# Kernel tuning notes

Measured on AMD Instinct MI355X. Metric: run time of the kernel, lower is better.

Reference implementation:

```python
import jax, jax.numpy as jnp
import numpy as np

M = 16          # max number of instance ids (0 = background)
DELTA_AGG = 0.5
DELTA_DIS = 3.0


def setup_inputs() -> dict:
    key = jax.random.key(0)
    k1, k2 = jax.random.split(key)
    preds = jax.random.normal(k1, (8, 6, 640, 640), dtype=jnp.float32)
    targets = jax.random.randint(k2, (8, 2, 640, 640), 0, M).astype(jnp.int32)
    return {"preds": preds, "targets": targets}


def _seg_sum(vals, ids):
    # vals: [P] or [P, C], ids: [P] -> segment sums with M segments
    return jax.ops.segment_sum(vals, ids, num_segments=M)


def reference(preds, targets):
    N = preds.shape[0]
    sim = preds[:, 2:, :, :].reshape(N, 4, -1).transpose(0, 2, 1)  # N x P x 4
    text = targets[:, 0].reshape(N, -1)                            # N x P
    kern = targets[:, 1].reshape(N, -1)                            # N x P
    P = sim.shape[1]

    seg = jax.vmap(_seg_sum)
    ones = jnp.ones((N, P), sim.dtype)
    cnt_k = seg(ones, kern)                         # N x M kernel pixel counts
    cnt_t = seg(ones, text)                         # N x M text pixel counts
    G = seg(sim, kern) / jnp.maximum(cnt_k, 1.0)[..., None]  # N x M x 4, G_Ki means

    inst = jnp.arange(M)
    valid = (cnt_k > 0) & (cnt_t > 0) & (inst[None, :] >= 1)  # N x M (skip id 0)
    nv = jnp.sum(valid, axis=1)                                # N, number of valid instances

    # ---- aggregation loss: per text pixel, distance to its instance's kernel mean
    G_t = jnp.take_along_axis(G, text[..., None], axis=1)      # N x P x 4
    d = jnp.linalg.norm(sim - G_t, axis=-1) - DELTA_AGG        # N x P
    l = jnp.log(jnp.square(jnp.maximum(d, 0.0)) + 1.0)         # N x P
    l_mean = seg(l, text) / jnp.maximum(cnt_t, 1.0)            # N x M per-instance mean
    agg = jnp.sum(jnp.where(valid, l_mean, 0.0), axis=1) / jnp.maximum(nv, 1)

    # ---- discrimination loss: pairwise distances between valid kernel means
    pair = valid[:, :, None] & valid[:, None, :] & ~jnp.eye(M, dtype=bool)[None]
    sq = jnp.sum(jnp.square(G[:, :, None, :] - G[:, None, :, :]), axis=-1)  # N x M x M
    dist = jnp.sqrt(jnp.where(pair, sq, 1.0))
    lp = jnp.where(pair, jnp.log(jnp.square(jnp.maximum(DELTA_DIS - dist, 0.0)) + 1.0), 0.0)
    dis = jnp.where(nv > 1, 0.5 * jnp.sum(lp, axis=(1, 2)) / jnp.maximum(nv * (nv - 1), 1), 0.0)

    return agg.astype(jnp.float32), dis.astype(jnp.float32)
```

## Files before the change

kernel.cpp:

```cpp
#include <hip/hip_runtime.h>
#include <math.h>

#define NB 8
#define MSEG 16
#define PPIX (640*640)
#define PV4 (PPIX/4)
#define DELTA_AGG 0.5f
#define DELTA_DIS 3.0f

#define OFF_CNT_K 0
#define OFF_CNT_T (NB*MSEG)
#define OFF_G     (2*NB*MSEG)
#define OFF_LSUM  (6*NB*MSEG)
#define WS_FLOATS (7*NB*MSEG)

__device__ __forceinline__ float wave_sum64(float v) {
#pragma unroll
  for (int off = 32; off > 0; off >>= 1) v += __shfl_xor(v, off);
  return v;
}

__global__ __launch_bounds__(256, 2) void pass1_kernel(
    const float* __restrict__ preds, const int* __restrict__ targets,
    float* __restrict__ ws) {
  const int n = blockIdx.y;
  const int tid = threadIdx.x;

  const float4* __restrict__ c0 = (const float4*)(preds + ((size_t)n*6 + 2)*PPIX);
  const float4* __restrict__ c1 = (const float4*)(preds + ((size_t)n*6 + 3)*PPIX);
  const float4* __restrict__ c2 = (const float4*)(preds + ((size_t)n*6 + 4)*PPIX);
  const float4* __restrict__ c3 = (const float4*)(preds + ((size_t)n*6 + 5)*PPIX);
  const int4*  __restrict__ textv = (const int4*)(targets + (size_t)n*2*PPIX);
  const int4*  __restrict__ kernv = (const int4*)(targets + ((size_t)n*2 + 1)*PPIX);

  float s0[MSEG], s1[MSEG], s2[MSEG], s3[MSEG], ck[MSEG], ct[MSEG];
#pragma unroll
  for (int m = 0; m < MSEG; ++m) { s0[m]=0.f; s1[m]=0.f; s2[m]=0.f; s3[m]=0.f; ck[m]=0.f; ct[m]=0.f; }

#define PIX1(K, T, A0, A1, A2, A3)                      \
  _Pragma("unroll")                                     \
  for (int m = 0; m < MSEG; ++m) {                      \
    float fk = ((K) == m) ? 1.0f : 0.0f;                \
    s0[m] = fmaf(fk, (A0), s0[m]);                      \
    s1[m] = fmaf(fk, (A1), s1[m]);                      \
    s2[m] = fmaf(fk, (A2), s2[m]);                      \
    s3[m] = fmaf(fk, (A3), s3[m]);                      \
    ck[m] += fk;                                        \
    ct[m] += ((T) == m) ? 1.0f : 0.0f;                  \
  }

  for (int p = blockIdx.x*256 + tid; p < PV4; p += gridDim.x*256) {
    int4 kk = kernv[p];
    int4 tt = textv[p];
    float4 a = c0[p], b = c1[p], c = c2[p], d = c3[p];
    PIX1(kk.x, tt.x, a.x, b.x, c.x, d.x);
    PIX1(kk.y, tt.y, a.y, b.y, c.y, d.y);
    PIX1(kk.z, tt.z, a.z, b.z, c.z, d.z);
    PIX1(kk.w, tt.w, a.w, b.w, c.w, d.w);
  }
#undef PIX1

#pragma unroll
  for (int m = 0; m < MSEG; ++m) {
    s0[m] = wave_sum64(s0[m]);
    s1[m] = wave_sum64(s1[m]);
    s2[m] = wave_sum64(s2[m]);
    s3[m] = wave_sum64(s3[m]);
    ck[m] = wave_sum64(ck[m]);
    ct[m] = wave_sum64(ct[m]);
  }

  __shared__ float s_red[4][96];
  const int w = tid >> 6, lane = tid & 63;
  if (lane == 0) {
#pragma unroll
    for (int m = 0; m < MSEG; ++m) {
      s_red[w][m*4 + 0] = s0[m];
      s_red[w][m*4 + 1] = s1[m];
      s_red[w][m*4 + 2] = s2[m];
      s_red[w][m*4 + 3] = s3[m];
      s_red[w][64 + m]  = ck[m];
      s_red[w][80 + m]  = ct[m];
    }
  }
  __syncthreads();
  if (tid < 96) {
    float v = s_red[0][tid] + s_red[1][tid] + s_red[2][tid] + s_red[3][tid];
    if (tid < 64)      atomicAdd(&ws[OFF_G + n*64 + tid], v);
    else if (tid < 80) atomicAdd(&ws[OFF_CNT_K + n*MSEG + (tid - 64)], v);
    else               atomicAdd(&ws[OFF_CNT_T + n*MSEG + (tid - 80)], v);
  }
}

__global__ __launch_bounds__(256) void finalize_dis_kernel(
    float* __restrict__ ws, float* __restrict__ out) {
  const int n = blockIdx.x;
  const int tid = threadIdx.x;
  float* cnt_k = ws + OFF_CNT_K + n*MSEG;
  float* cnt_t = ws + OFF_CNT_T + n*MSEG;
  float* G     = ws + OFF_G     + (size_t)n*MSEG*4;

  __shared__ float s_G[MSEG][4];
  __shared__ int   s_valid[MSEG];
  __shared__ int   s_nv;
  __shared__ float red[256];

  if (tid < MSEG*4) {
    int m = tid >> 2;
    float g = G[tid] / fmaxf(cnt_k[m], 1.0f);
    s_G[m][tid & 3] = g;
    G[tid] = g;
  }
  if (tid < MSEG)
    s_valid[tid] = (tid >= 1) && (cnt_k[tid] > 0.f) && (cnt_t[tid] > 0.f);
  __syncthreads();
  if (tid == 0) { int nv = 0; for (int m = 0; m < MSEG; m++) nv += s_valid[m]; s_nv = nv; }

  float lp = 0.f;
  {
    int i = tid >> 4, j = tid & 15;
    if (i != j && s_valid[i] && s_valid[j]) {
      float dx = s_G[i][0] - s_G[j][0];
      float dy = s_G[i][1] - s_G[j][1];
      float dz = s_G[i][2] - s_G[j][2];
      float dw = s_G[i][3] - s_G[j][3];
      float dist = sqrtf(dx*dx + dy*dy + dz*dz + dw*dw);
      float t = fmaxf(DELTA_DIS - dist, 0.f);
      lp = logf(t*t + 1.f);
    }
  }
  red[tid] = lp;
  __syncthreads();
  for (int s = 128; s > 0; s >>= 1) {
    if (tid < s) red[tid] += red[tid + s];
    __syncthreads();
  }
  if (tid == 0) {
    int nv = s_nv;
    float dis = 0.f;
    if (nv > 1) dis = 0.5f * red[0] / (float)(nv * (nv - 1));
    out[NB + n] = dis;
  }
}

__global__ __launch_bounds__(256, 2) void pass2_kernel(
    const float* __restrict__ preds, const int* __restrict__ targets,
    float* __restrict__ ws) {
  const int n = blockIdx.y;
  const int tid = threadIdx.x;

  const float4* __restrict__ c0 = (const float4*)(preds + ((size_t)n*6 + 2)*PPIX);
  const float4* __restrict__ c1 = (const float4*)(preds + ((size_t)n*6 + 3)*PPIX);
  const float4* __restrict__ c2 = (const float4*)(preds + ((size_t)n*6 + 4)*PPIX);
  const float4* __restrict__ c3 = (const float4*)(preds + ((size_t)n*6 + 5)*PPIX);
  const int4*  __restrict__ textv = (const int4*)(targets + (size_t)n*2*PPIX);

  __shared__ float4 s_G[MSEG];
  if (tid < MSEG) s_G[tid] = ((const float4*)(ws + OFF_G + (size_t)n*MSEG*4))[tid];
  __syncthreads();

  float ls[MSEG];
#pragma unroll
  for (int m = 0; m < MSEG; ++m) ls[m] = 0.f;

#define PIX2(T, A0, A1, A2, A3) do {                            \
    float4 g = s_G[(T)];                                        \
    float dx = (A0) - g.x, dy = (A1) - g.y;                     \
    float dz = (A2) - g.z, dw = (A3) - g.w;                     \
    float sq = fmaf(dx, dx, fmaf(dy, dy, fmaf(dz, dz, dw*dw))); \
    float dd = fmaxf(__fsqrt_rn(sq) - DELTA_AGG, 0.f);          \
    float l = __logf(fmaf(dd, dd, 1.f));                        \
    _Pragma("unroll")                                           \
    for (int m = 0; m < MSEG; ++m)                              \
      ls[m] += ((T) == m) ? l : 0.f;                            \
  } while (0)

  for (int p = blockIdx.x*256 + tid; p < PV4; p += gridDim.x*256) {
    int4 tt = textv[p];
    float4 a = c0[p], b = c1[p], c = c2[p], d = c3[p];
    PIX2(tt.x, a.x, b.x, c.x, d.x);
    PIX2(tt.y, a.y, b.y, c.y, d.y);
    PIX2(tt.z, a.z, b.z, c.z, d.z);
    PIX2(tt.w, a.w, b.w, c.w, d.w);
  }
#undef PIX2

#pragma unroll
  for (int m = 0; m < MSEG; ++m) ls[m] = wave_sum64(ls[m]);

  __shared__ float s_red[4][MSEG];
  const int w = tid >> 6, lane = tid & 63;
  if (lane == 0) {
#pragma unroll
    for (int m = 0; m < MSEG; ++m) s_red[w][m] = ls[m];
  }
  __syncthreads();
  if (tid < MSEG) {
    float v = s_red[0][tid] + s_red[1][tid] + s_red[2][tid] + s_red[3][tid];
    atomicAdd(&ws[OFF_LSUM + n*MSEG + tid], v);
  }
}

__global__ __launch_bounds__(64) void finalize_agg_kernel(
    const float* __restrict__ ws, float* __restrict__ out) {
  const int n = blockIdx.x;
  const int tid = threadIdx.x;
  const float* cnt_k = ws + OFF_CNT_K + n*MSEG;
  const float* cnt_t = ws + OFF_CNT_T + n*MSEG;
  const float* lsum  = ws + OFF_LSUM  + n*MSEG;

  float lm = 0.f, vc = 0.f;
  if (tid >= 1 && tid < MSEG) {
    float ck = cnt_k[tid], ct = cnt_t[tid];
    if (ck > 0.f && ct > 0.f) {
      vc = 1.f;
      lm = lsum[tid] / fmaxf(ct, 1.f);
    }
  }
  for (int off = 32; off > 0; off >>= 1) {
    lm += __shfl_down(lm, off);
    vc += __shfl_down(vc, off);
  }
  if (tid == 0) {
    int nv = (int)(vc + 0.5f);
    out[n] = lm / (float)(nv > 1 ? nv : 1);
  }
}

extern "C" void kernel_launch(void* const* d_in, const int* in_sizes, int n_in,
                              void* d_out, int out_size, void* d_ws, size_t ws_size,
                              hipStream_t stream) {
  const float* preds   = (const float*)d_in[0];
  const int*   targets = (const int*)d_in[1];
  float* out = (float*)d_out;
  float* ws  = (float*)d_ws;

  hipMemsetAsync(d_ws, 0, WS_FLOATS * sizeof(float), stream);

  dim3 grid(128, NB);
  pass1_kernel<<<grid, 256, 0, stream>>>(preds, targets, ws);
  finalize_dis_kernel<<<NB, 256, 0, stream>>>(ws, out);
  pass2_kernel<<<grid, 256, 0, stream>>>(preds, targets, ws);
  finalize_agg_kernel<<<NB, 64, 0, stream>>>(ws, out);
}
```

Baseline: 67.32 us.

## Use ballot counts, transpose-style wave reductions and fixed-trip unrolled loops

Pass 1 now counts kernel and text pixels with wave ballots plus popcount instead of per-lane float counters, which removes 32 accumulator registers. Both passes replace per-segment butterfly wave sums with a recursive-halving reduction that shuffles half the accumulators at each step, so the total number of shuffles drops. The grid is reduced to 100 blocks so each thread does exactly 4 fully unrolled iterations. This hardcodes the image size divisibility (100*256*4 == PV4) and raises instruction-level parallelism, at some register pressure cost.

Result: slower. 160.5 us (+138.4%).

```diff
diff --git a/kernel.cpp b/kernel.cpp
--- a/kernel.cpp
+++ b/kernel.cpp
@@ -5,6 +5,8 @@
 #define MSEG 16
 #define PPIX (640*640)
 #define PV4 (PPIX/4)
+#define GRIDX 100
+#define STRIDE (GRIDX*256)
 #define DELTA_AGG 0.5f
 #define DELTA_DIS 3.0f
 
@@ -14,17 +16,12 @@
 #define OFF_LSUM  (6*NB*MSEG)
 #define WS_FLOATS (7*NB*MSEG)
 
-__device__ __forceinline__ float wave_sum64(float v) {
-#pragma unroll
-  for (int off = 32; off > 0; off >>= 1) v += __shfl_xor(v, off);
-  return v;
-}
-
 __global__ __launch_bounds__(256, 2) void pass1_kernel(
     const float* __restrict__ preds, const int* __restrict__ targets,
     float* __restrict__ ws) {
   const int n = blockIdx.y;
   const int tid = threadIdx.x;
+  const int lane = tid & 63, w = tid >> 6;
 
   const float4* __restrict__ c0 = (const float4*)(preds + ((size_t)n*6 + 2)*PPIX);
   const float4* __restrict__ c1 = (const float4*)(preds + ((size_t)n*6 + 3)*PPIX);
@@ -33,23 +30,30 @@
   const int4*  __restrict__ textv = (const int4*)(targets + (size_t)n*2*PPIX);
   const int4*  __restrict__ kernv = (const int4*)(targets + ((size_t)n*2 + 1)*PPIX);
 
-  float s0[MSEG], s1[MSEG], s2[MSEG], s3[MSEG], ck[MSEG], ct[MSEG];
-#pragma unroll
-  for (int m = 0; m < MSEG; ++m) { s0[m]=0.f; s1[m]=0.f; s2[m]=0.f; s3[m]=0.f; ck[m]=0.f; ct[m]=0.f; }
-
-#define PIX1(K, T, A0, A1, A2, A3)                      \
-  _Pragma("unroll")                                     \
-  for (int m = 0; m < MSEG; ++m) {                      \
-    float fk = ((K) == m) ? 1.0f : 0.0f;                \
-    s0[m] = fmaf(fk, (A0), s0[m]);                      \
-    s1[m] = fmaf(fk, (A1), s1[m]);                      \
-    s2[m] = fmaf(fk, (A2), s2[m]);                      \
-    s3[m] = fmaf(fk, (A3), s3[m]);                      \
-    ck[m] += fk;                                        \
-    ct[m] += ((T) == m) ? 1.0f : 0.0f;                  \
-  }
-
-  for (int p = blockIdx.x*256 + tid; p < PV4; p += gridDim.x*256) {
+  float vals[64];
+#pragma unroll
+  for (int v = 0; v < 64; ++v) vals[v] = 0.f;
+  int ckw[MSEG], ctw[MSEG];
+#pragma unroll
+  for (int m = 0; m < MSEG; ++m) { ckw[m] = 0; ctw[m] = 0; }
+
+#define PIX1(K, T, A0, A1, A2, A3)                                  \
+  _Pragma("unroll")                                                 \
+  for (int m = 0; m < MSEG; ++m) {                                  \
+    bool pk = ((K) == m);                                           \
+    ckw[m] += __popcll(__ballot(pk));                               \
+    ctw[m] += __popcll(__ballot((T) == m));                         \
+    float fk = pk ? 1.0f : 0.0f;                                    \
+    vals[0*16+m] = fmaf(fk, (A0), vals[0*16+m]);                    \
+    vals[1*16+m] = fmaf(fk, (A1), vals[1*16+m]);                    \
+    vals[2*16+m] = fmaf(fk, (A2), vals[2*16+m]);                    \
+    vals[3*16+m] = fmaf(fk, (A3), vals[3*16+m]);                    \
+  }
+
+  const int base = blockIdx.x*256 + tid;
+#pragma unroll
+  for (int it = 0; it < 4; ++it) {
+    int p = base + it*STRIDE;
     int4 kk = kernv[p];
     int4 tt = textv[p];
     float4 a = c0[p], b = c1[p], c = c2[p], d = c3[p];
@@ -61,34 +65,34 @@
 #undef PIX1
 
 #pragma unroll
-  for (int m = 0; m < MSEG; ++m) {
-    s0[m] = wave_sum64(s0[m]);
-    s1[m] = wave_sum64(s1[m]);
-    s2[m] = wave_sum64(s2[m]);
-    s3[m] = wave_sum64(s3[m]);
-    ck[m] = wave_sum64(ck[m]);
-    ct[m] = wave_sum64(ct[m]);
-  }
-
-  __shared__ float s_red[4][96];
-  const int w = tid >> 6, lane = tid & 63;
+  for (int s = 0; s < 6; ++s) {
+    const int dist = 32 >> s;
+    const bool hi = (lane & dist) != 0;
+#pragma unroll
+    for (int v = 0; v < (32 >> s); ++v) {
+      float keep = hi ? vals[v + (32 >> s)] : vals[v];
+      float send = hi ? vals[v] : vals[v + (32 >> s)];
+      vals[v] = keep + __shfl_xor(send, dist);
+    }
+  }
+
+  __shared__ float s_vals[4][64];
+  __shared__ int   s_cnt[4][32];
+  s_vals[w][lane] = vals[0];
   if (lane == 0) {
 #pragma unroll
-    for (int m = 0; m < MSEG; ++m) {
-      s_red[w][m*4 + 0] = s0[m];
-      s_red[w][m*4 + 1] = s1[m];
-      s_red[w][m*4 + 2] = s2[m];
-      s_red[w][m*4 + 3] = s3[m];
-      s_red[w][64 + m]  = ck[m];
-      s_red[w][80 + m]  = ct[m];
-    }
-  }
-  __syncthreads();
-  if (tid < 96) {
-    float v = s_red[0][tid] + s_red[1][tid] + s_red[2][tid] + s_red[3][tid];
-    if (tid < 64)      atomicAdd(&ws[OFF_G + n*64 + tid], v);
-    else if (tid < 80) atomicAdd(&ws[OFF_CNT_K + n*MSEG + (tid - 64)], v);
-    else               atomicAdd(&ws[OFF_CNT_T + n*MSEG + (tid - 80)], v);
+    for (int m = 0; m < MSEG; ++m) { s_cnt[w][m] = ckw[m]; s_cnt[w][16+m] = ctw[m]; }
+  }
+  __syncthreads();
+  if (tid < 64) {
+    float v = s_vals[0][tid] + s_vals[1][tid] + s_vals[2][tid] + s_vals[3][tid];
+    int ch = tid >> 4, m = tid & 15;
+    atomicAdd(&ws[OFF_G + n*64 + m*4 + ch], v);
+  } else if (tid < 96) {
+    int i = tid - 64;
+    float v = (float)(s_cnt[0][i] + s_cnt[1][i] + s_cnt[2][i] + s_cnt[3][i]);
+    if (i < 16) atomicAdd(&ws[OFF_CNT_K + n*MSEG + i], v);
+    else        atomicAdd(&ws[OFF_CNT_T + n*MSEG + (i - 16)], v);
   }
 }
 
@@ -148,6 +152,7 @@
     float* __restrict__ ws) {
   const int n = blockIdx.y;
   const int tid = threadIdx.x;
+  const int lane = tid & 63, w = tid >> 6;
 
   const float4* __restrict__ c0 = (const float4*)(preds + ((size_t)n*6 + 2)*PPIX);
   const float4* __restrict__ c1 = (const float4*)(preds + ((size_t)n*6 + 3)*PPIX);
@@ -175,7 +180,10 @@
       ls[m] += ((T) == m) ? l : 0.f;                            \
   } while (0)
 
-  for (int p = blockIdx.x*256 + tid; p < PV4; p += gridDim.x*256) {
+  const int base = blockIdx.x*256 + tid;
+#pragma unroll
+  for (int it = 0; it < 4; ++it) {
+    int p = base + it*STRIDE;
     int4 tt = textv[p];
     float4 a = c0[p], b = c1[p], c = c2[p], d = c3[p];
     PIX2(tt.x, a.x, b.x, c.x, d.x);
@@ -186,19 +194,26 @@
 #undef PIX2
 
 #pragma unroll
-  for (int m = 0; m < MSEG; ++m) ls[m] = wave_sum64(ls[m]);
+  for (int s = 0; s < 4; ++s) {
+    const int dist = 32 >> s;
+    const bool hi = (lane & dist) != 0;
+#pragma unroll
+    for (int v = 0; v < (8 >> s); ++v) {
+      float keep = hi ? ls[v + (8 >> s)] : ls[v];
+      float send = hi ? ls[v] : ls[v + (8 >> s)];
+      ls[v] = keep + __shfl_xor(send, dist);
+    }
+  }
+  float t = ls[0];
+  t += __shfl_xor(t, 2);
+  t += __shfl_xor(t, 1);
 
   __shared__ float s_red[4][MSEG];
-  const int w = tid >> 6, lane = tid & 63;
-  if (lane == 0) {
-#pragma unroll
-    for (int m = 0; m < MSEG; ++m) s_red[w][m] = ls[m];
-  }
-  __syncthreads();
-  if (tid < MSEG) {
-    float v = s_red[0][tid] + s_red[1][tid] + s_red[2][tid] + s_red[3][tid];
-    atomicAdd(&ws[OFF_LSUM + n*MSEG + tid], v);
-  }
+  if ((lane & 3) == 0) s_red[w][lane >> 2] = t;
+  __syncthreads();
+  if (tid < MSEG)
+    atomicAdd(&ws[OFF_LSUM + n*MSEG + tid],
+              s_red[0][tid] + s_red[1][tid] + s_red[2][tid] + s_red[3][tid]);
 }
 
 __global__ __launch_bounds__(64) void finalize_agg_kernel(
@@ -237,7 +252,7 @@
 
   hipMemsetAsync(d_ws, 0, WS_FLOATS * sizeof(float), stream);
 
-  dim3 grid(128, NB);
+  dim3 grid(GRIDX, NB);
   pass1_kernel<<<grid, 256, 0, stream>>>(preds, targets, ws);
   finalize_dis_kernel<<<NB, 256, 0, stream>>>(ws, out);
   pass2_kernel<<<grid, 256, 0, stream>>>(preds, targets, ws);
```

## Replace register one-hot segment sums with LDS atomic histograms

Applied to the files above, without the earlier changes.

Both passes drop the per-thread 16-way one-hot accumulation across 96 (pass1) or 16 (pass2) registers. Each pixel now does shared-memory atomicAdds into per-column bins, with pairs of threads sharing a column. At the end, threads reduce the rows and issue global atomics. The grid becomes a fixed 100 blocks per image, each covering exactly 1024 float4s with no grid-stride loop. This cuts ALU work and register pressure, but adds contention on LDS float atomics and depends on the exact size match (100*1024 == PV4).

Result: slower. 174.6 us (+159.4%).

```diff
diff --git a/kernel.cpp b/kernel.cpp
--- a/kernel.cpp
+++ b/kernel.cpp
@@ -5,6 +5,7 @@
 #define MSEG 16
 #define PPIX (640*640)
 #define PV4 (PPIX/4)
+#define GRIDX 100
 #define DELTA_AGG 0.5f
 #define DELTA_DIS 3.0f
 
@@ -14,17 +15,12 @@
 #define OFF_LSUM  (6*NB*MSEG)
 #define WS_FLOATS (7*NB*MSEG)
 
-__device__ __forceinline__ float wave_sum64(float v) {
-#pragma unroll
-  for (int off = 32; off > 0; off >>= 1) v += __shfl_xor(v, off);
-  return v;
-}
-
-__global__ __launch_bounds__(256, 2) void pass1_kernel(
+__global__ __launch_bounds__(256) void pass1_kernel(
     const float* __restrict__ preds, const int* __restrict__ targets,
     float* __restrict__ ws) {
   const int n = blockIdx.y;
   const int tid = threadIdx.x;
+  const int col = tid >> 1;
 
   const float4* __restrict__ c0 = (const float4*)(preds + ((size_t)n*6 + 2)*PPIX);
   const float4* __restrict__ c1 = (const float4*)(preds + ((size_t)n*6 + 3)*PPIX);
@@ -33,23 +29,28 @@
   const int4*  __restrict__ textv = (const int4*)(targets + (size_t)n*2*PPIX);
   const int4*  __restrict__ kernv = (const int4*)(targets + ((size_t)n*2 + 1)*PPIX);
 
-  float s0[MSEG], s1[MSEG], s2[MSEG], s3[MSEG], ck[MSEG], ct[MSEG];
-#pragma unroll
-  for (int m = 0; m < MSEG; ++m) { s0[m]=0.f; s1[m]=0.f; s2[m]=0.f; s3[m]=0.f; ck[m]=0.f; ct[m]=0.f; }
-
-#define PIX1(K, T, A0, A1, A2, A3)                      \
-  _Pragma("unroll")                                     \
-  for (int m = 0; m < MSEG; ++m) {                      \
-    float fk = ((K) == m) ? 1.0f : 0.0f;                \
-    s0[m] = fmaf(fk, (A0), s0[m]);                      \
-    s1[m] = fmaf(fk, (A1), s1[m]);                      \
-    s2[m] = fmaf(fk, (A2), s2[m]);                      \
-    s3[m] = fmaf(fk, (A3), s3[m]);                      \
-    ck[m] += fk;                                        \
-    ct[m] += ((T) == m) ? 1.0f : 0.0f;                  \
-  }
-
-  for (int p = blockIdx.x*256 + tid; p < PV4; p += gridDim.x*256) {
+  __shared__ float s_acc[6][MSEG][128];
+  {
+    float4* f4 = (float4*)&s_acc[0][0][0];
+#pragma unroll
+    for (int i = 0; i < 12; ++i) f4[tid + i*256] = make_float4(0.f, 0.f, 0.f, 0.f);
+  }
+  __syncthreads();
+
+#define PIX1(K, T, A0, A1, A2, A3) do {          \
+    int k_ = (K), t_ = (T);                      \
+    atomicAdd(&s_acc[0][k_][col], (A0));         \
+    atomicAdd(&s_acc[1][k_][col], (A1));         \
+    atomicAdd(&s_acc[2][k_][col], (A2));         \
+    atomicAdd(&s_acc[3][k_][col], (A3));         \
+    atomicAdd(&s_acc[4][k_][col], 1.0f);         \
+    atomicAdd(&s_acc[5][t_][col], 1.0f);         \
+  } while (0)
+
+  const int base = blockIdx.x*1024 + tid;
+#pragma unroll
+  for (int it = 0; it < 4; ++it) {
+    int p = base + it*256;
     int4 kk = kernv[p];
     int4 tt = textv[p];
     float4 a = c0[p], b = c1[p], c = c2[p], d = c3[p];
@@ -59,36 +60,20 @@
     PIX1(kk.w, tt.w, a.w, b.w, c.w, d.w);
   }
 #undef PIX1
-
-#pragma unroll
-  for (int m = 0; m < MSEG; ++m) {
-    s0[m] = wave_sum64(s0[m]);
-    s1[m] = wave_sum64(s1[m]);
-    s2[m] = wave_sum64(s2[m]);
-    s3[m] = wave_sum64(s3[m]);
-    ck[m] = wave_sum64(ck[m]);
-    ct[m] = wave_sum64(ct[m]);
-  }
-
-  __shared__ float s_red[4][96];
-  const int w = tid >> 6, lane = tid & 63;
-  if (lane == 0) {
-#pragma unroll
-    for (int m = 0; m < MSEG; ++m) {
-      s_red[w][m*4 + 0] = s0[m];
-      s_red[w][m*4 + 1] = s1[m];
-      s_red[w][m*4 + 2] = s2[m];
-      s_red[w][m*4 + 3] = s3[m];
-      s_red[w][64 + m]  = ck[m];
-      s_red[w][80 + m]  = ct[m];
-    }
-  }
-  __syncthreads();
+  __syncthreads();
+
   if (tid < 96) {
-    float v = s_red[0][tid] + s_red[1][tid] + s_red[2][tid] + s_red[3][tid];
-    if (tid < 64)      atomicAdd(&ws[OFF_G + n*64 + tid], v);
-    else if (tid < 80) atomicAdd(&ws[OFF_CNT_K + n*MSEG + (tid - 64)], v);
-    else               atomicAdd(&ws[OFF_CNT_T + n*MSEG + (tid - 80)], v);
+    const int arr = tid >> 4, bin = tid & 15;
+    const float4* row = (const float4*)&s_acc[arr][bin][0];
+    float s = 0.f;
+#pragma unroll
+    for (int i = 0; i < 32; ++i) {
+      float4 v = row[i];
+      s += (v.x + v.y) + (v.z + v.w);
+    }
+    if (arr < 4)       atomicAdd(&ws[OFF_G + n*64 + bin*4 + arr], s);
+    else if (arr == 4) atomicAdd(&ws[OFF_CNT_K + n*MSEG + bin], s);
+    else               atomicAdd(&ws[OFF_CNT_T + n*MSEG + bin], s);
   }
 }
 
@@ -143,11 +128,12 @@
   }
 }
 
-__global__ __launch_bounds__(256, 2) void pass2_kernel(
+__global__ __launch_bounds__(256) void pass2_kernel(
     const float* __restrict__ preds, const int* __restrict__ targets,
     float* __restrict__ ws) {
   const int n = blockIdx.y;
   const int tid = threadIdx.x;
+  const int col = tid >> 1;
 
   const float4* __restrict__ c0 = (const float4*)(preds + ((size_t)n*6 + 2)*PPIX);
   const float4* __restrict__ c1 = (const float4*)(preds + ((size_t)n*6 + 3)*PPIX);
@@ -156,26 +142,30 @@
   const int4*  __restrict__ textv = (const int4*)(targets + (size_t)n*2*PPIX);
 
   __shared__ float4 s_G[MSEG];
+  __shared__ float  s_l[MSEG][128];
   if (tid < MSEG) s_G[tid] = ((const float4*)(ws + OFF_G + (size_t)n*MSEG*4))[tid];
-  __syncthreads();
-
-  float ls[MSEG];
-#pragma unroll
-  for (int m = 0; m < MSEG; ++m) ls[m] = 0.f;
+  {
+    float4* f4 = (float4*)&s_l[0][0];
+#pragma unroll
+    for (int i = 0; i < 2; ++i) f4[tid + i*256] = make_float4(0.f, 0.f, 0.f, 0.f);
+  }
+  __syncthreads();
 
 #define PIX2(T, A0, A1, A2, A3) do {                            \
-    float4 g = s_G[(T)];                                        \
+    int t_ = (T);                                               \
+    float4 g = s_G[t_];                                         \
     float dx = (A0) - g.x, dy = (A1) - g.y;                     \
     float dz = (A2) - g.z, dw = (A3) - g.w;                     \
     float sq = fmaf(dx, dx, fmaf(dy, dy, fmaf(dz, dz, dw*dw))); \
     float dd = fmaxf(__fsqrt_rn(sq) - DELTA_AGG, 0.f);          \
     float l = __logf(fmaf(dd, dd, 1.f));                        \
-    _Pragma("unroll")                                           \
-    for (int m = 0; m < MSEG; ++m)                              \
-      ls[m] += ((T) == m) ? l : 0.f;                            \
+    atomicAdd(&s_l[t_][col], l);                                \
   } while (0)
 
-  for (int p = blockIdx.x*256 + tid; p < PV4; p += gridDim.x*256) {
+  const int base = blockIdx.x*1024 + tid;
+#pragma unroll
+  for (int it = 0; it < 4; ++it) {
+    int p = base + it*256;
     int4 tt = textv[p];
     float4 a = c0[p], b = c1[p], c = c2[p], d = c3[p];
     PIX2(tt.x, a.x, b.x, c.x, d.x);
@@ -184,20 +174,17 @@
     PIX2(tt.w, a.w, b.w, c.w, d.w);
   }
 #undef PIX2
-
-#pragma unroll
-  for (int m = 0; m < MSEG; ++m) ls[m] = wave_sum64(ls[m]);
-
-  __shared__ float s_red[4][MSEG];
-  const int w = tid >> 6, lane = tid & 63;
-  if (lane == 0) {
-#pragma unroll
-    for (int m = 0; m < MSEG; ++m) s_red[w][m] = ls[m];
-  }
-  __syncthreads();
+  __syncthreads();
+
   if (tid < MSEG) {
-    float v = s_red[0][tid] + s_red[1][tid] + s_red[2][tid] + s_red[3][tid];
-    atomicAdd(&ws[OFF_LSUM + n*MSEG + tid], v);
+    const float4* row = (const float4*)&s_l[tid][0];
+    float s = 0.f;
+#pragma unroll
+    for (int i = 0; i < 32; ++i) {
+      float4 v = row[i];
+      s += (v.x + v.y) + (v.z + v.w);
+    }
+    atomicAdd(&ws[OFF_LSUM + n*MSEG + tid], s);
   }
 }
 
@@ -237,7 +224,7 @@
 
   hipMemsetAsync(d_ws, 0, WS_FLOATS * sizeof(float), stream);
 
-  dim3 grid(128, NB);
+  dim3 grid(GRIDX, NB);
   pass1_kernel<<<grid, 256, 0, stream>>>(preds, targets, ws);
   finalize_dis_kernel<<<NB, 256, 0, stream>>>(ws, out);
   pass2_kernel<<<grid, 256, 0, stream>>>(preds, targets, ws);
```
